# Kernel optimization log

Hardware: AMD Instinct MI355X
Metric: run time of the kernel (lower is better)

## Reference

```python
import jax, jax.numpy as jnp
import numpy as np

DIM = 1024
DIM_HEAD = 64
HEADS = 16
DIM_INNER = DIM_HEAD * HEADS  # 1024


def setup_inputs() -> dict:
    key = jax.random.key(0)
    k1, k2, k3 = jax.random.split(key, 3)
    b, n = 2, 2048
    x = jax.random.normal(k1, (b, n, DIM), dtype=jnp.float32)
    gamma = jnp.ones((DIM,), dtype=jnp.float32)
    # torch Linear weight [out,in] applied as x @ W.T; store pre-transposed [in,out]
    w_qkv = jax.random.normal(k2, (DIM, 3 * DIM_INNER), dtype=jnp.float32) * (DIM ** -0.5)
    w_out = jax.random.normal(k3, (DIM_INNER, DIM), dtype=jnp.float32) * (DIM_INNER ** -0.5)
    return {"x": x, "gamma": gamma, "w_qkv": w_qkv, "w_out": w_out}


def reference(x, gamma, w_qkv, w_out):
    h, d = HEADS, DIM_HEAD
    scale = d ** -0.5
    rms_scale = DIM ** 0.5
    # RMSNorm: F.normalize(x, dim=-1) * sqrt(dim) * gamma  (eps=1e-12 clamp on L2 norm)
    norm = jnp.maximum(jnp.linalg.norm(x, axis=-1, keepdims=True), 1e-12)
    xn = x / norm * rms_scale * gamma
    b, n, _ = x.shape
    qkv = xn @ w_qkv  # [b, n, 3*h*d]
    qkv = qkv.reshape(b, n, 3, h, d)
    q = qkv[:, :, 0].transpose(0, 2, 1, 3) * scale  # [b, h, n, d]
    k = qkv[:, :, 1].transpose(0, 2, 1, 3)
    v = qkv[:, :, 2].transpose(0, 2, 1, 3)
    sim = jnp.einsum('bhid,bhjd->bhij', q, k)  # [b, h, n, n]
    causal_mask = jnp.triu(jnp.ones((n, n), dtype=bool), k=1)
    neg = -jnp.finfo(sim.dtype).max
    sim = jnp.where(causal_mask, neg, sim)
    attn = jax.nn.softmax(sim, axis=-1)
    out = jnp.einsum('bhij,bhjd->bhid', attn, v)  # [b, h, n, d]
    out = out.transpose(0, 2, 1, 3).reshape(b, n, h * d)
    return out @ w_out
```

## Files before the change

### kernel.cpp

```cpp
#include <hip/hip_runtime.h>
#include <hip/hip_bf16.h>

typedef __bf16 bf16x8 __attribute__((ext_vector_type(8)));
typedef short s16x4 __attribute__((ext_vector_type(4)));
typedef short s16x8 __attribute__((ext_vector_type(8)));
typedef float f32x4 __attribute__((ext_vector_type(4)));
typedef unsigned short u16x8 __attribute__((ext_vector_type(8)));

#define MFMA_K32(a, b, c) __builtin_amdgcn_mfma_f32_16x16x32_bf16(a, b, c, 0, 0, 0)

static __device__ __forceinline__ f32x4 mfma_k16(s16x4 a, s16x4 b, f32x4 c) {
#ifdef __HIP_DEVICE_COMPILE__
    return __builtin_amdgcn_mfma_f32_16x16x16bf16_1k(a, b, c, 0, 0, 0);
#else
    return c;
#endif
}

static __device__ __forceinline__ float fast_exp2(float x) {
#ifdef __HIP_DEVICE_COMPILE__
    return __builtin_amdgcn_exp2f(x);
#else
    return x;
#endif
}

#define GLL16(gp, lp)                                              \
    __builtin_amdgcn_global_load_lds(                              \
        (const __attribute__((address_space(1))) void*)(gp),       \
        (__attribute__((address_space(3))) void*)(lp), 16, 0, 0)

static __device__ __forceinline__ unsigned short f2bf(float f) {
    unsigned int u = __float_as_uint(f);
    u += 0x7fffu + ((u >> 16) & 1u);
    return (unsigned short)(u >> 16);
}

static __device__ __forceinline__ unsigned int cvtpk_bf16(float lo, float hi) {
#if defined(__HIP_DEVICE_COMPILE__) && __has_builtin(__builtin_amdgcn_cvt_pk_bf16_f32)
    typedef __bf16 bf16x2 __attribute__((ext_vector_type(2)));
    bf16x2 r = __builtin_amdgcn_cvt_pk_bf16_f32(lo, hi);
    return __builtin_bit_cast(unsigned int, r);
#else
    return (unsigned int)f2bf(lo) | ((unsigned int)f2bf(hi) << 16);
#endif
}

#define LOG2E 1.44269504088896340736f

__global__ __launch_bounds__(256) void prep_k(
    const float* __restrict__ x, const float* __restrict__ gamma,
    const float* __restrict__ w_qkv, const float* __restrict__ w_out,
    unsigned short* __restrict__ xn, unsigned short* __restrict__ wtq,
    unsigned short* __restrict__ wto) {
    __shared__ float sm[32][33];
    int bid = blockIdx.x, tid = threadIdx.x;
    if (bid < 4096) {
        const float* in;
        unsigned short* out;
        int R = 1024, C, bx, by;
        if (bid < 3072) { in = w_qkv; out = wtq; C = 3072; bx = bid % 96; by = bid / 96; }
        else { int b2 = bid - 3072; in = w_out; out = wto; C = 1024; bx = b2 % 32; by = b2 / 32; }
        int c0 = bx * 32, r0 = by * 32;
        int tr = tid >> 5, tc = tid & 31;
#pragma unroll
        for (int i = 0; i < 4; i++)
            sm[tr + i * 8][tc] = in[(size_t)(r0 + tr + i * 8) * C + c0 + tc];
        __syncthreads();
#pragma unroll
        for (int i = 0; i < 4; i++)
            out[(size_t)(c0 + tr + i * 8) * R + r0 + tc] = f2bf(sm[tc][tr + i * 8]);
    } else {
        int row = bid - 4096;
        const float* xr = x + (size_t)row * 1024;
        float4 v = *(const float4*)(xr + tid * 4);
        float ss = v.x * v.x + v.y * v.y + v.z * v.z + v.w * v.w;
#pragma unroll
        for (int off = 1; off < 64; off <<= 1) ss += __shfl_xor(ss, off, 64);
        if ((tid & 63) == 0) sm[0][tid >> 6] = ss;
        __syncthreads();
        float tot = sm[0][0] + sm[0][1] + sm[0][2] + sm[0][3];
        float f = 32.0f / fmaxf(sqrtf(tot), 1e-12f);
        float4 g = *(const float4*)(gamma + tid * 4);
        uint2 o;
        o.x = cvtpk_bf16(v.x * f * g.x, v.y * f * g.y);
        o.y = cvtpk_bf16(v.z * f * g.z, v.w * f * g.w);
        *(uint2*)(xn + (size_t)row * 1024 + tid * 4) = o;
    }
}

template <int MODE, int BM>
__global__ __launch_bounds__(256) void gemm_bt_k(
    const unsigned short* __restrict__ A, const unsigned short* __restrict__ BT,
    float* __restrict__ C, unsigned short* __restrict__ qw,
    unsigned short* __restrict__ kw, unsigned short* __restrict__ vw,
    int M, int N, int K) {
    constexpr int RT = 4;
    constexpr int CT = (BM == 128) ? 4 : 2;
    __shared__ unsigned short As[BM][32];
    __shared__ unsigned short Bs[128][32];
    int tid = threadIdx.x;
    int wave = tid >> 6, lane = tid & 63, quad = lane >> 4, l16 = lane & 15;
    int wrb, wcb;
    if constexpr (BM == 128) { wrb = (wave >> 1) * 64; wcb = (wave & 1) * 64; }
    else { wrb = 0; wcb = wave * 32; }
    int m0 = blockIdx.y * BM, n0 = blockIdx.x * 128;
    int lrow = lane >> 2, lcol = (lane & 3) * 8;
    const unsigned short *Ag0, *Ag1 = nullptr;
    if constexpr (BM == 128) {
        Ag0 = A + (size_t)(m0 + wave * 32 + lrow) * K + lcol;
        Ag1 = A + (size_t)(m0 + wave * 32 + 16 + lrow) * K + lcol;
    } else {
        Ag0 = A + (size_t)(m0 + wave * 16 + lrow) * K + lcol;
    }
    const unsigned short* Bg0 = BT + (size_t)(n0 + wave * 32 + lrow) * K + lcol;
    const unsigned short* Bg1 = BT + (size_t)(n0 + wave * 32 + 16 + lrow) * K + lcol;
    f32x4 acc[RT][CT] = {};
    for (int k0 = 0; k0 < K; k0 += 32) {
        __syncthreads();
        if constexpr (BM == 128) {
            GLL16(Ag0 + k0, &As[wave * 32][0]);
            GLL16(Ag1 + k0, &As[wave * 32 + 16][0]);
        } else {
            GLL16(Ag0 + k0, &As[wave * 16][0]);
        }
        GLL16(Bg0 + k0, &Bs[wave * 32][0]);
        GLL16(Bg1 + k0, &Bs[wave * 32 + 16][0]);
        __syncthreads();
        bf16x8 af[RT], bfr[CT];
#pragma unroll
        for (int t = 0; t < RT; t++)
            af[t] = *(const bf16x8*)&As[wrb + t * 16 + l16][quad * 8];
#pragma unroll
        for (int t = 0; t < CT; t++)
            bfr[t] = *(const bf16x8*)&Bs[wcb + t * 16 + l16][quad * 8];
#pragma unroll
        for (int rt = 0; rt < RT; rt++)
#pragma unroll
            for (int ct = 0; ct < CT; ct++)
                acc[rt][ct] = MFMA_K32(af[rt], bfr[ct], acc[rt][ct]);
    }
#pragma unroll
    for (int rt = 0; rt < RT; rt++) {
        int mb = m0 + wrb + rt * 16 + quad * 4;
#pragma unroll
        for (int ct = 0; ct < CT; ct++) {
            int col = n0 + wcb + ct * 16 + l16;
            if (MODE == 0) {
#pragma unroll
                for (int r = 0; r < 4; r++)
                    C[(size_t)(mb + r) * N + col] = acc[rt][ct][r];
            } else {
                int sec = mb >> 10, ci = mb & 1023;
                int hh = ci >> 6, ddb = ci & 63;
                int bb = col >> 11, t = col & 2047;
                int bh = bb * 16 + hh;
                if (sec == 0) {
                    uint2 pk;
                    pk.x = cvtpk_bf16(acc[rt][ct][0] * (0.125f * LOG2E),
                                      acc[rt][ct][1] * (0.125f * LOG2E));
                    pk.y = cvtpk_bf16(acc[rt][ct][2] * (0.125f * LOG2E),
                                      acc[rt][ct][3] * (0.125f * LOG2E));
                    *(uint2*)&qw[((size_t)bh * 2048 + t) * 64 + ddb] = pk;
                } else if (sec == 1) {
                    uint2 pk;
                    pk.x = cvtpk_bf16(acc[rt][ct][0], acc[rt][ct][1]);
                    pk.y = cvtpk_bf16(acc[rt][ct][2], acc[rt][ct][3]);
                    *(uint2*)&kw[((size_t)bh * 2048 + t) * 64 + ddb] = pk;
                } else {
                    int sb = (t & ~63) | (((t >> 2) & 3) << 4) |
                             (((t >> 4) & 3) << 2) | (t & 3);
#pragma unroll
                    for (int r = 0; r < 4; r++)
                        vw[((size_t)bh * 64 + ddb + r) * 2048 + sb] =
                            f2bf(acc[rt][ct][r]);
                }
            }
        }
    }
}

__global__ __launch_bounds__(256, 2) void attn_k(
    const unsigned short* __restrict__ q, const unsigned short* __restrict__ k,
    const unsigned short* __restrict__ vt, unsigned short* __restrict__ o,
    int* __restrict__ counter) {
    __shared__ unsigned short Ks[2][128][72];
    __shared__ unsigned short Vt[2][64][136];
    __shared__ int item_sh;
    int tid = threadIdx.x, wave = tid >> 6, lane = tid & 63;
    int quad = lane >> 4, l16 = lane & 15;
    int krow = tid >> 1, kcol = (tid & 1) * 32;
    int vrow = tid >> 2, vcol = (tid & 3) * 32;
    for (;;) {
        if (tid == 0) item_sh = atomicAdd(counter, 1);
        __syncthreads();
        int item = item_sh;
        if (item >= 1024) break;
        int qt = 31 - (item >> 5);
        int bh = item & 31;
        int b = bh >> 4, h = bh & 15;
        const unsigned short* qg = q + (size_t)bh * 2048 * 64;
        const unsigned short* kg = k + (size_t)bh * 2048 * 64;
        const unsigned short* vg = vt + (size_t)bh * 64 * 2048;
        int q0w = qt * 64 + wave * 16;
        bf16x8 bq[2];
#pragma unroll
        for (int ks = 0; ks < 2; ks++)
            bq[ks] = *(const bf16x8*)&qg[(size_t)(q0w + l16) * 64 + ks * 32 + quad * 8];
        f32x4 ot[4] = {};
        float mrun = -1e38f, lrun = 0.f;
        int nkt = (qt >> 1) + 1;
        u16x8 pk[4], pv[4];
        {
            const unsigned short* kp = kg + (size_t)krow * 64 + kcol;
            const unsigned short* vp = vg + (size_t)vrow * 2048 + vcol;
#pragma unroll
            for (int i = 0; i < 4; i++) {
                pk[i] = *(const u16x8*)(kp + i * 8);
                pv[i] = *(const u16x8*)(vp + i * 8);
            }
#pragma unroll
            for (int i = 0; i < 4; i++) {
                *(u16x8*)&Ks[0][krow][kcol + i * 8] = pk[i];
                *(u16x8*)&Vt[0][vrow][vcol + i * 8] = pv[i];
            }
        }
        __syncthreads();
        for (int kt = 0; kt < nkt; kt++) {
            int cb = kt & 1;
            bool pf = (kt + 1 < nkt);
            if (pf) {
                const unsigned short* kp = kg + (size_t)((kt + 1) * 128 + krow) * 64 + kcol;
                const unsigned short* vp = vg + (size_t)vrow * 2048 + (kt + 1) * 128 + vcol;
#pragma unroll
                for (int i = 0; i < 4; i++) {
                    pk[i] = *(const u16x8*)(kp + i * 8);
                    pv[i] = *(const u16x8*)(vp + i * 8);
                }
            }
            f32x4 sf[8];
#pragma unroll
            for (int ct = 0; ct < 8; ct++) {
                bf16x8 ak0 = *(const bf16x8*)&Ks[cb][ct * 16 + l16][quad * 8];
                bf16x8 ak1 = *(const bf16x8*)&Ks[cb][ct * 16 + l16][32 + quad * 8];
                f32x4 s = {};
                s = MFMA_K32(ak0, bq[0], s);
                s = MFMA_K32(ak1, bq[1], s);
                sf[ct] = s;
            }
            if (kt == nkt - 1) {
                int qrow = q0w + l16;
                int keyb = kt * 128 + quad * 4;
#pragma unroll
                for (int ct = 0; ct < 8; ct++)
#pragma unroll
                    for (int r = 0; r < 4; r++)
                        if (keyb + ct * 16 + r > qrow) sf[ct][r] = -1e30f;
            }
            float mx = -1e30f;
#pragma unroll
            for (int ct = 0; ct < 8; ct++)
#pragma unroll
                for (int r = 0; r < 4; r++) mx = fmaxf(mx, sf[ct][r]);
            mx = fmaxf(mx, __shfl_xor(mx, 16, 64));
            mx = fmaxf(mx, __shfl_xor(mx, 32, 64));
            float mnew = fmaxf(mrun, mx);
            float al = fast_exp2(mrun - mnew);
            mrun = mnew;
            float rs = 0.f;
#pragma unroll
            for (int ct = 0; ct < 8; ct++)
#pragma unroll
                for (int r = 0; r < 4; r++) {
                    float p = fast_exp2(sf[ct][r] - mnew);
                    sf[ct][r] = p;
                    rs += p;
                }
            rs += __shfl_xor(rs, 16, 64);
            rs += __shfl_xor(rs, 32, 64);
            lrun = lrun * al + rs;
            s16x4 bpr[8];
#pragma unroll
            for (int ct = 0; ct < 8; ct++) {
                uint2 u;
                u.x = cvtpk_bf16(sf[ct][0], sf[ct][1]);
                u.y = cvtpk_bf16(sf[ct][2], sf[ct][3]);
                bpr[ct] = __builtin_bit_cast(s16x4, u);
            }
            if (__any(al < 1.0f)) {
#pragma unroll
                for (int dt = 0; dt < 4; dt++)
#pragma unroll
                    for (int r = 0; r < 4; r++) ot[dt][r] *= al;
            }
#pragma unroll
            for (int dt = 0; dt < 4; dt++) {
#pragma unroll
                for (int blk = 0; blk < 2; blk++)
#pragma unroll
                    for (int p = 0; p < 2; p++) {
                        s16x8 av = *(const s16x8*)&Vt[cb][dt * 16 + l16]
                                                      [blk * 64 + quad * 16 + p * 8];
                        s16x4 lo = __builtin_shufflevector(av, av, 0, 1, 2, 3);
                        s16x4 hi = __builtin_shufflevector(av, av, 4, 5, 6, 7);
                        int ct = blk * 4 + p * 2;
                        ot[dt] = mfma_k16(lo, bpr[ct], ot[dt]);
                        ot[dt] = mfma_k16(hi, bpr[ct + 1], ot[dt]);
                    }
            }
            if (pf) {
#pragma unroll
                for (int i = 0; i < 4; i++) {
                    *(u16x8*)&Ks[1 - cb][krow][kcol + i * 8] = pk[i];
                    *(u16x8*)&Vt[1 - cb][vrow][vcol + i * 8] = pv[i];
                }
            }
            __syncthreads();
        }
        float inv = 1.0f / lrun;
        size_t rowbase = ((size_t)b * 2048 + q0w + l16) * 1024 + h * 64;
#pragma unroll
        for (int dt = 0; dt < 4; dt++) {
            uint2 pk2;
            pk2.x = cvtpk_bf16(ot[dt][0] * inv, ot[dt][1] * inv);
            pk2.y = cvtpk_bf16(ot[dt][2] * inv, ot[dt][3] * inv);
            *(uint2*)&o[rowbase + dt * 16 + quad * 4] = pk2;
        }
    }
}

extern "C" void kernel_launch(void* const* d_in, const int* in_sizes, int n_in,
                              void* d_out, int out_size, void* d_ws, size_t ws_size,
                              hipStream_t stream) {
    const float* x = (const float*)d_in[0];
    const float* gamma = (const float*)d_in[1];
    const float* w_qkv = (const float*)d_in[2];
    const float* w_out = (const float*)d_in[3];
    float* out = (float*)d_out;
    char* ws = (char*)d_ws;

    unsigned short* xn = (unsigned short*)(ws);
    unsigned short* wtq = (unsigned short*)(ws + 8388608);
    unsigned short* wto = (unsigned short*)(ws + 14680064);
    unsigned short* qw = (unsigned short*)(ws + 16777216);
    unsigned short* kw = (unsigned short*)(ws + 25165824);
    unsigned short* vw = (unsigned short*)(ws + 33554432);
    unsigned short* ao = xn;
    int* counter = (int*)(ws + 8388608);

    prep_k<<<8192, 256, 0, stream>>>(x, gamma, w_qkv, w_out, xn, wtq, wto);
    gemm_bt_k<2, 128><<<dim3(32, 24), 256, 0, stream>>>(wtq, xn, nullptr, qw, kw, vw,
                                                        3072, 4096, 1024);
    hipMemsetAsync(counter, 0, 4, stream);
    attn_k<<<512, 256, 0, stream>>>(qw, kw, vw, ao, counter);
    gemm_bt_k<0, 64><<<dim3(8, 64), 256, 0, stream>>>(ao, wto, out, nullptr, nullptr,
                                                      nullptr, 4096, 1024, 1024);
}
```

Before: 194.8 us.

## Load V fragments directly from global into registers, raise attention occupancy

The attention kernel no longer stages transposed V tiles through shared memory. Each lane loads its V operand fragments directly from global memory into registers before the PV matmul. This halves LDS use and lets launch bounds target three blocks per CU. The work-counter reset moves into the prep kernel, stored in the output buffer, removing a separate memset. The cost is less latency hiding for the V loads and higher register pressure.

Result: slower. 243.7 us (+25.1%).

```diff
diff --git a/kernel.cpp b/kernel.cpp
--- a/kernel.cpp
+++ b/kernel.cpp
@@ -52,9 +52,10 @@
     const float* __restrict__ x, const float* __restrict__ gamma,
     const float* __restrict__ w_qkv, const float* __restrict__ w_out,
     unsigned short* __restrict__ xn, unsigned short* __restrict__ wtq,
-    unsigned short* __restrict__ wto) {
+    unsigned short* __restrict__ wto, int* __restrict__ counter) {
     __shared__ float sm[32][33];
     int bid = blockIdx.x, tid = threadIdx.x;
+    if (bid == 0 && tid == 0) *counter = 0;
     if (bid < 4096) {
         const float* in;
         unsigned short* out;
@@ -180,17 +181,15 @@
     }
 }
 
-__global__ __launch_bounds__(256, 2) void attn_k(
+__global__ __launch_bounds__(256, 3) void attn_k(
     const unsigned short* __restrict__ q, const unsigned short* __restrict__ k,
     const unsigned short* __restrict__ vt, unsigned short* __restrict__ o,
     int* __restrict__ counter) {
     __shared__ unsigned short Ks[2][128][72];
-    __shared__ unsigned short Vt[2][64][136];
     __shared__ int item_sh;
     int tid = threadIdx.x, wave = tid >> 6, lane = tid & 63;
     int quad = lane >> 4, l16 = lane & 15;
     int krow = tid >> 1, kcol = (tid & 1) * 32;
-    int vrow = tid >> 2, vcol = (tid & 3) * 32;
     for (;;) {
         if (tid == 0) item_sh = atomicAdd(counter, 1);
         __syncthreads();
@@ -210,20 +209,13 @@
         f32x4 ot[4] = {};
         float mrun = -1e38f, lrun = 0.f;
         int nkt = (qt >> 1) + 1;
-        u16x8 pk[4], pv[4];
+        u16x8 pk[4];
         {
             const unsigned short* kp = kg + (size_t)krow * 64 + kcol;
-            const unsigned short* vp = vg + (size_t)vrow * 2048 + vcol;
-#pragma unroll
-            for (int i = 0; i < 4; i++) {
-                pk[i] = *(const u16x8*)(kp + i * 8);
-                pv[i] = *(const u16x8*)(vp + i * 8);
-            }
-#pragma unroll
-            for (int i = 0; i < 4; i++) {
-                *(u16x8*)&Ks[0][krow][kcol + i * 8] = pk[i];
-                *(u16x8*)&Vt[0][vrow][vcol + i * 8] = pv[i];
-            }
+#pragma unroll
+            for (int i = 0; i < 4; i++) pk[i] = *(const u16x8*)(kp + i * 8);
+#pragma unroll
+            for (int i = 0; i < 4; i++) *(u16x8*)&Ks[0][krow][kcol + i * 8] = pk[i];
         }
         __syncthreads();
         for (int kt = 0; kt < nkt; kt++) {
@@ -231,12 +223,8 @@
             bool pf = (kt + 1 < nkt);
             if (pf) {
                 const unsigned short* kp = kg + (size_t)((kt + 1) * 128 + krow) * 64 + kcol;
-                const unsigned short* vp = vg + (size_t)vrow * 2048 + (kt + 1) * 128 + vcol;
-#pragma unroll
-                for (int i = 0; i < 4; i++) {
-                    pk[i] = *(const u16x8*)(kp + i * 8);
-                    pv[i] = *(const u16x8*)(vp + i * 8);
-                }
+#pragma unroll
+                for (int i = 0; i < 4; i++) pk[i] = *(const u16x8*)(kp + i * 8);
             }
             f32x4 sf[8];
 #pragma unroll
@@ -247,6 +235,17 @@
                 s = MFMA_K32(ak0, bq[0], s);
                 s = MFMA_K32(ak1, bq[1], s);
                 sf[ct] = s;
+            }
+            s16x8 av[4][2][2];
+#pragma unroll
+            for (int dt = 0; dt < 4; dt++) {
+                const unsigned short* vr = vg + (size_t)(dt * 16 + l16) * 2048 + kt * 128;
+#pragma unroll
+                for (int blk = 0; blk < 2; blk++)
+#pragma unroll
+                    for (int p = 0; p < 2; p++)
+                        av[dt][blk][p] =
+                            *(const s16x8*)(vr + blk * 64 + quad * 16 + p * 8);
             }
             if (kt == nkt - 1) {
                 int qrow = q0w + l16;
@@ -299,10 +298,9 @@
                 for (int blk = 0; blk < 2; blk++)
 #pragma unroll
                     for (int p = 0; p < 2; p++) {
-                        s16x8 av = *(const s16x8*)&Vt[cb][dt * 16 + l16]
-                                                      [blk * 64 + quad * 16 + p * 8];
-                        s16x4 lo = __builtin_shufflevector(av, av, 0, 1, 2, 3);
-                        s16x4 hi = __builtin_shufflevector(av, av, 4, 5, 6, 7);
+                        s16x8 a8 = av[dt][blk][p];
+                        s16x4 lo = __builtin_shufflevector(a8, a8, 0, 1, 2, 3);
+                        s16x4 hi = __builtin_shufflevector(a8, a8, 4, 5, 6, 7);
                         int ct = blk * 4 + p * 2;
                         ot[dt] = mfma_k16(lo, bpr[ct], ot[dt]);
                         ot[dt] = mfma_k16(hi, bpr[ct + 1], ot[dt]);
@@ -310,10 +308,8 @@
             }
             if (pf) {
 #pragma unroll
-                for (int i = 0; i < 4; i++) {
+                for (int i = 0; i < 4; i++)
                     *(u16x8*)&Ks[1 - cb][krow][kcol + i * 8] = pk[i];
-                    *(u16x8*)&Vt[1 - cb][vrow][vcol + i * 8] = pv[i];
-                }
             }
             __syncthreads();
         }
@@ -346,12 +342,11 @@
     unsigned short* kw = (unsigned short*)(ws + 25165824);
     unsigned short* vw = (unsigned short*)(ws + 33554432);
     unsigned short* ao = xn;
-    int* counter = (int*)(ws + 8388608);
-
-    prep_k<<<8192, 256, 0, stream>>>(x, gamma, w_qkv, w_out, xn, wtq, wto);
+    int* counter = (int*)d_out;
+
+    prep_k<<<8192, 256, 0, stream>>>(x, gamma, w_qkv, w_out, xn, wtq, wto, counter);
     gemm_bt_k<2, 128><<<dim3(32, 24), 256, 0, stream>>>(wtq, xn, nullptr, qw, kw, vw,
                                                         3072, 4096, 1024);
-    hipMemsetAsync(counter, 0, 4, stream);
     attn_k<<<512, 256, 0, stream>>>(qw, kw, vw, ao, counter);
     gemm_bt_k<0, 64><<<dim3(8, 64), 256, 0, stream>>>(ao, wto, out, nullptr, nullptr,
                                                       nullptr, 4096, 1024, 1024);
```
